# Kernel tuning notes

Hardware: AMD Instinct MI355X
Metric: run time of the kernel (lower is better)

The kernel has to match this reference:

```python
import jax, jax.numpy as jnp
import numpy as np

B, S = 1, 2048
HIDDEN = 2560
NH, NKV, HD = 32, 8, 128
GS = 128  # awq group size
ROPE_THETA = 1000000.0


def dequant_q4(qweight, scales, qzeros):
    """Unpack int4 AWQ weights -> dense [K, N] float weight.
    qweight: [K//8, N] int32, 8 nibbles packed along the input (K) dim.
    scales/qzeros: [K//GS, N]. w = (nibble - zero) * scale.
    """
    K8, N = qweight.shape
    shifts = jnp.arange(8, dtype=jnp.int32) * 4
    nib = (qweight[:, None, :] >> shifts[None, :, None]) & 0xF  # [K//8, 8, N]
    w = nib.reshape(K8 * 8, N).astype(scales.dtype)             # [K, N]
    z = jnp.repeat(qzeros.astype(scales.dtype), GS, axis=0)     # [K, N]
    s = jnp.repeat(scales, GS, axis=0)                          # [K, N]
    return (w - z) * s


def linear_q4(x, qw, sc, qz, bias=None):
    w = dequant_q4(qw, sc, qz)                     # [K, N]
    y = jnp.einsum('bsk,kn->bsn', x, w)
    return y + bias if bias is not None else y


def rotate_half(x):
    x1, x2 = jnp.split(x, 2, axis=-1)
    return jnp.concatenate([-x2, x1], axis=-1)


def apply_rope(q, k, cos, sin):
    # cos/sin: [B, S, HD] -> broadcast over heads at dim 2
    c = cos[:, :, None, :]
    s = sin[:, :, None, :]
    return q * c + rotate_half(q) * s, k * c + rotate_half(k) * s


def setup_inputs() -> dict:
    key = jax.random.key(0)
    ks = jax.random.split(key, 12)

    x = jax.random.normal(ks[0], (B, S, HIDDEN), dtype=jnp.float32)

    # genuine rotary embedding tables
    inv_freq = 1.0 / (ROPE_THETA ** (np.arange(0, HD, 2, dtype=np.float32) / HD))
    t = np.arange(S, dtype=np.float32)
    freqs = np.outer(t, inv_freq)                      # [S, HD/2]
    emb = np.concatenate([freqs, freqs], axis=-1)      # [S, HD]
    cos = jnp.asarray(np.cos(emb)[None], dtype=jnp.float32)  # [1, S, HD]
    sin = jnp.asarray(np.sin(emb)[None], dtype=jnp.float32)

    def mk_proj(kq, ksc, kz, K, N, group=GS):
        qw = jax.random.randint(kq, (K // 8, N), 0, 2**31 - 1, dtype=jnp.int32)
        sc = jax.random.normal(ksc, (K // group, N), dtype=jnp.float32) * 0.01
        qz = jax.random.randint(kz, (K // group, N), 0, 16, dtype=jnp.int32)
        return qw, sc, qz

    q_qweight, q_scales, q_qzeros = mk_proj(ks[1], ks[2], ks[3], HIDDEN, NH * HD)
    k_qweight, k_scales, k_qzeros = mk_proj(ks[4], ks[5], ks[6], HIDDEN, NKV * HD)
    v_qweight, v_scales, v_qzeros = mk_proj(ks[7], ks[8], ks[9], HIDDEN, NKV * HD)
    o_qweight, o_scales, o_qzeros = mk_proj(ks[10], ks[11], jax.random.fold_in(key, 99), NH * HD, HIDDEN)

    kb = jax.random.split(jax.random.fold_in(key, 7), 3)
    q_bias = jax.random.normal(kb[0], (NH * HD,), dtype=jnp.float32) * 0.02
    k_bias = jax.random.normal(kb[1], (NKV * HD,), dtype=jnp.float32) * 0.02
    v_bias = jax.random.normal(kb[2], (NKV * HD,), dtype=jnp.float32) * 0.02

    return dict(x=x, cos=cos, sin=sin,
                q_scales=q_scales, q_bias=q_bias,
                k_scales=k_scales, k_bias=k_bias,
                v_scales=v_scales, v_bias=v_bias,
                o_scales=o_scales,
                q_qweight=q_qweight, q_qzeros=q_qzeros,
                k_qweight=k_qweight, k_qzeros=k_qzeros,
                v_qweight=v_qweight, v_qzeros=v_qzeros,
                o_qweight=o_qweight, o_qzeros=o_qzeros)


def reference(x, cos, sin,
              q_scales, q_bias, k_scales, k_bias, v_scales, v_bias, o_scales,
              q_qweight, q_qzeros, k_qweight, k_qzeros,
              v_qweight, v_qzeros, o_qweight, o_qzeros):
    b, s, _ = x.shape
    xq = linear_q4(x, q_qweight, q_scales, q_qzeros, q_bias).reshape(b, s, NH, HD)
    xk = linear_q4(x, k_qweight, k_scales, k_qzeros, k_bias).reshape(b, s, NKV, HD)
    xv = linear_q4(x, v_qweight, v_scales, v_qzeros, v_bias).reshape(b, s, NKV, HD)

    xq, xk = apply_rope(xq, xk, cos, sin)

    # GQA: repeat KV heads to match query heads (prefill, start_pos=0)
    rep = NH // NKV
    xk = jnp.repeat(xk, rep, axis=2)   # [b, s, NH, HD]
    xv = jnp.repeat(xv, rep, axis=2)

    scale = 1.0 / jnp.sqrt(jnp.asarray(HD, dtype=xq.dtype))
    scores = jnp.einsum('bqhd,bkhd->bhqk', xq, xk) * scale  # [b, NH, s, s]
    causal = jnp.tril(jnp.ones((s, s), dtype=bool))
    scores = jnp.where(causal[None, None], scores, jnp.finfo(scores.dtype).min)
    attn = jax.nn.softmax(scores, axis=-1)
    out = jnp.einsum('bhqk,bkhd->bqhd', attn, xv).reshape(b, s, NH * HD)

    return linear_q4(out, o_qweight, o_scales, o_qzeros)  # [b, s, HIDDEN]
```

## Files before the change

### kernel.cpp

```cpp
#include <hip/hip_runtime.h>
#include <hip/hip_bf16.h>
#include <cstdint>

#define S_LEN 2048
#define HIDDEN 2560
#define NH 32
#define NKV 8
#define HD 128
#define GS 128

typedef __attribute__((ext_vector_type(8))) _Float16 half8v;
typedef __attribute__((ext_vector_type(2))) _Float16 half2v;
typedef __attribute__((ext_vector_type(4))) float f32x4;
typedef unsigned int uint;
typedef unsigned short ushort;

__device__ inline ushort f2h(float f) {
    _Float16 h = (_Float16)f;
    return __builtin_bit_cast(ushort, h);
}
__device__ inline float h2f(ushort u) {
    return (float)__builtin_bit_cast(_Float16, u);
}
__device__ inline uint pk2(ushort a, ushort b) { return (uint)a | ((uint)b << 16); }

__device__ __attribute__((always_inline)) inline void gl_lds16(const void* g, void* l) {
    __builtin_amdgcn_global_load_lds(
        (const __attribute__((address_space(1))) unsigned int*)g,
        (__attribute__((address_space(3))) unsigned int*)l, 16, 0, 0);
}

#define WAIT_LGKM0  asm volatile("s_waitcnt lgkmcnt(0)" ::: "memory")
#define WAIT_VM(N)  asm volatile("s_waitcnt vmcnt(" #N ")" ::: "memory")
#define RAW_BARRIER { __builtin_amdgcn_s_barrier(); __builtin_amdgcn_sched_barrier(0); }

__global__ __launch_bounds__(320) void xcvt_kernel(
    const float* __restrict__ X, ushort* __restrict__ Xf)
{
    const int row = blockIdx.x;
    const int t   = threadIdx.x;
    const size_t base = (size_t)row * HIDDEN + t * 8;
    float4 a = *(const float4*)&X[base];
    float4 b = *(const float4*)&X[base + 4];
    uint4 hw = {pk2(f2h(a.x), f2h(a.y)), pk2(f2h(a.z), f2h(a.w)),
                pk2(f2h(b.x), f2h(b.y)), pk2(f2h(b.z), f2h(b.w))};
    *(uint4*)&Xf[base] = hw;
}

__global__ __launch_bounds__(256) void qkv7_kernel(
    const ushort* __restrict__ Xf,
    const int* __restrict__ q_qw, const float* __restrict__ q_sc,
    const int* __restrict__ q_qz, const float* __restrict__ q_b,
    const int* __restrict__ k_qw, const float* __restrict__ k_sc,
    const int* __restrict__ k_qz, const float* __restrict__ k_b,
    const int* __restrict__ v_qw, const float* __restrict__ v_sc,
    const int* __restrict__ v_qz, const float* __restrict__ v_b,
    const float* __restrict__ cosb, const float* __restrict__ sinb,
    ushort* __restrict__ Qf, ushort* __restrict__ Kf,
    ushort* __restrict__ Vrm)
{
    __shared__ __align__(16) char LDSB[65536];
    ushort* A0 = (ushort*)(LDSB);
    ushort* A1 = (ushort*)(LDSB + 16384);
    ushort* B0 = (ushort*)(LDSB + 32768);
    ushort* B1 = (ushort*)(LDSB + 49152);

    const int t  = threadIdx.x;
    const int w  = t >> 6;
    const int l  = t & 63;
    const int lg = l >> 4;
    const int lr = l & 15;
    const int wr = w >> 1;
    const int wc = w & 1;
    const int K  = HIDDEN;

    const int bid = blockIdx.x;
    const int swz = (bid & 7) * 96 + (bid >> 3);
    const int nblk = swz % 48;
    const int m0   = (swz / 48) * 128;

    int region, nbase, Nw;
    const int* QW; const float* SC; const int* QZ; const float* BI;
    if (nblk < 32)      { region = 0; nbase = nblk * 128;        Nw = NH * HD;
                          QW = q_qw; SC = q_sc; QZ = q_qz; BI = q_b; }
    else if (nblk < 40) { region = 1; nbase = (nblk - 32) * 128; Nw = NKV * HD;
                          QW = k_qw; SC = k_sc; QZ = k_qz; BI = k_b; }
    else                { region = 2; nbase = (nblk - 40) * 128; Nw = NKV * HD;
                          QW = v_qw; SC = v_sc; QZ = v_qz; BI = v_b; }

    const int ldsAw = w * 1024;
    size_t aoff[4];
#pragma unroll
    for (int i = 0; i < 4; ++i) {
        int slot = i * 256 + t;
        int am = slot >> 3, ac = slot & 7;
        aoff[i] = (size_t)(m0 + am) * K + (size_t)((ac ^ (am & 7)) * 8);
    }
    const int bn  = t & 127;
    const int bk0 = (t >> 7) * 4;
    int bwoff[4];
#pragma unroll
    for (int j = 0; j < 4; ++j)
        bwoff[j] = (bn * 128 + (bk0 + j) * 16) ^ ((bn & 7) << 4);

    int ncm[4];
#pragma unroll
    for (int nf = 0; nf < 4; ++nf)
        ncm[nf] = wc * 32 + (nf & 1) * 16 + lr + ((nf & 2) ? 64 : 0);

    const int xorA = (lr & 7) << 4;
    int aroff[4][2], broff[4][2];
#pragma unroll
    for (int mf = 0; mf < 4; ++mf)
#pragma unroll
        for (int ks = 0; ks < 2; ++ks)
            aroff[mf][ks] = (((wr * 64 + mf * 16 + lr) * 128) + lg * 16 + ks * 64) ^ xorA;
#pragma unroll
    for (int nf = 0; nf < 4; ++nf)
#pragma unroll
        for (int ks = 0; ks < 2; ++ks)
            broff[nf][ks] = ((ncm[nf] * 128) + lg * 16 + ks * 64) ^ xorA;

    f32x4 macc[4][4];
#pragma unroll
    for (int mf = 0; mf < 4; ++mf)
#pragma unroll
        for (int nf = 0; nf < 4; ++nf) macc[mf][nf] = f32x4{0.f, 0.f, 0.f, 0.f};
    uint qr[4];
    float scf, zf;

#define QKV_QW(tile) { int g8 = (tile) * 8; int gg = (tile) >> 1; \
    _Pragma("unroll") \
    for (int j = 0; j < 4; ++j) \
        qr[j] = (uint)QW[(size_t)(g8 + bk0 + j) * Nw + nbase + bn]; \
    scf = SC[(size_t)gg * Nw + nbase + bn]; \
    zf  = (float)QZ[(size_t)gg * Nw + nbase + bn]; }

#define QKV_STAGE_A(AH, k0) { \
    gl_lds16(Xf + (k0) + aoff[0], (char*)(AH) + ldsAw); \
    gl_lds16(Xf + (k0) + aoff[1], (char*)(AH) + 4096 + ldsAw); \
    gl_lds16(Xf + (k0) + aoff[2], (char*)(AH) + 8192 + ldsAw); \
    gl_lds16(Xf + (k0) + aoff[3], (char*)(AH) + 12288 + ldsAw); }

#define QKV_BWRITE(BT) { \
    ushort sch = f2h(scf); \
    float schf = h2f(sch); \
    ushort msc = f2h(-128.0f * schf);    \
    ushort nzs = f2h(-(zf * schf)); \
    half2v S2 = {__builtin_bit_cast(_Float16, sch), __builtin_bit_cast(_Float16, sch)}; \
    half2v M2 = {__builtin_bit_cast(_Float16, msc), __builtin_bit_cast(_Float16, msc)}; \
    half2v Z2 = {__builtin_bit_cast(_Float16, nzs), __builtin_bit_cast(_Float16, nzs)}; \
    _Pragma("unroll") \
    for (int j = 0; j < 4; ++j) { \
        uint q = qr[j]; \
        uint b0 = q & 0xFFu, b1 = (q >> 8) & 0xFFu, b2 = (q >> 16) & 0xFFu, b3 = q >> 24; \
        uint e0 = 0x58005800u | ((b0 & 0xFu) << 3) | ((b0 & 0xF0u) << 15); \
        uint e1 = 0x58005800u | ((b1 & 0xFu) << 3) | ((b1 & 0xF0u) << 15); \
        uint e2 = 0x58005800u | ((b2 & 0xFu) << 3) | ((b2 & 0xF0u) << 15); \
        uint e3 = 0x58005800u | ((b3 & 0xFu) << 3) | ((b3 & 0xF0u) << 15); \
        half2v w0 = __builtin_bit_cast(half2v, e0) * S2 + M2; w0 = w0 + Z2; \
        half2v w1 = __builtin_bit_cast(half2v, e1) * S2 + M2; w1 = w1 + Z2; \
        half2v w2 = __builtin_bit_cast(half2v, e2) * S2 + M2; w2 = w2 + Z2; \
        half2v w3 = __builtin_bit_cast(half2v, e3) * S2 + M2; w3 = w3 + Z2; \
        uint4 dw = {__builtin_bit_cast(uint, w0), __builtin_bit_cast(uint, w1), \
                    __builtin_bit_cast(uint, w2), __builtin_bit_cast(uint, w3)}; \
        *(uint4*)((char*)(BT) + bwoff[j]) = dw; \
    } }

#define QKV_COMPUTE(AH, BT) { \
    _Pragma("unroll") \
    for (int ks = 0; ks < 2; ++ks) { \
        half8v av[4], bv[4]; \
        _Pragma("unroll") \
        for (int mf = 0; mf < 4; ++mf) \
            av[mf] = *(const half8v*)((const char*)(AH) + aroff[mf][ks]); \
        _Pragma("unroll") \
        for (int nf = 0; nf < 4; ++nf) \
            bv[nf] = *(const half8v*)((const char*)(BT) + broff[nf][ks]); \
        _Pragma("unroll") \
        for (int mf = 0; mf < 4; ++mf) \
            _Pragma("unroll") \
            for (int nf = 0; nf < 4; ++nf) \
                macc[mf][nf] = __builtin_amdgcn_mfma_f32_16x16x32_f16(av[mf], bv[nf], macc[mf][nf], 0, 0, 0); \
    } }

    QKV_QW(0);
    QKV_BWRITE(B0);
    QKV_STAGE_A(A0, 0);
    QKV_QW(1);
    WAIT_LGKM0;
    WAIT_VM(6);
    RAW_BARRIER;

    for (int g = 0; g < 19; ++g) {
        QKV_STAGE_A(A1, (2 * g + 1) * 64);
        QKV_COMPUTE(A0, B0);
        QKV_BWRITE(B1);
        QKV_QW(2 * g + 2);
        WAIT_LGKM0;
        WAIT_VM(6);
        RAW_BARRIER;
        QKV_STAGE_A(A0, (2 * g + 2) * 64);
        QKV_COMPUTE(A1, B1);
        QKV_BWRITE(B0);
        QKV_QW(2 * g + 3);
        WAIT_LGKM0;
        WAIT_VM(6);
        RAW_BARRIER;
    }
    QKV_STAGE_A(A1, 39 * 64);
    QKV_COMPUTE(A0, B0);
    QKV_BWRITE(B1);
    WAIT_LGKM0;
    WAIT_VM(0);
    RAW_BARRIER;
    QKV_COMPUTE(A1, B1);

#pragma unroll
    for (int nf = 0; nf < 4; ++nf) {
        float bv = BI[nbase + ncm[nf]];
#pragma unroll
        for (int mf = 0; mf < 4; ++mf)
#pragma unroll
            for (int r = 0; r < 4; ++r) macc[mf][nf][r] += bv;
    }

    if (region == 2) {
#pragma unroll
        for (int mf = 0; mf < 4; ++mf)
#pragma unroll
            for (int r = 0; r < 4; ++r) {
                int row = m0 + wr * 64 + mf * 16 + lg * 4 + r;
#pragma unroll
                for (int nf = 0; nf < 4; ++nf)
                    Vrm[(size_t)row * (NKV * HD) + nbase + ncm[nf]] = f2h(macc[mf][nf][r]);
            }
    } else {
        ushort* OF = (region == 0) ? Qf : Kf;
        const int No = (region == 0) ? NH * HD : NKV * HD;
        const float osc = (region == 0) ? 0.08838834764831845f : 1.0f;
#pragma unroll
        for (int mf = 0; mf < 4; ++mf)
#pragma unroll
            for (int r = 0; r < 4; ++r) {
                int row = m0 + wr * 64 + mf * 16 + lg * 4 + r;
                const float* cb = &cosb[(size_t)row * HD];
                const float* sb = &sinb[(size_t)row * HD];
#pragma unroll
                for (int nf = 0; nf < 2; ++nf) {
                    int d = wc * 32 + nf * 16 + lr;
                    float a = macc[mf][nf][r];
                    float b = macc[mf][nf + 2][r];
                    float o1 = (a * cb[d]      - b * sb[d])      * osc;
                    float o2 = (b * cb[d + 64] + a * sb[d + 64]) * osc;
                    OF[(size_t)row * No + nbase + d]      = f2h(o1);
                    OF[(size_t)row * No + nbase + d + 64] = f2h(o2);
                }
            }
    }
#undef QKV_QW
#undef QKV_STAGE_A
#undef QKV_BWRITE
#undef QKV_COMPUTE
}

__global__ __launch_bounds__(256) void vtrans_kernel(
    const ushort* __restrict__ Vrm, ushort* __restrict__ VfT)
{
    __shared__ ushort Ts[64][65];
    const int s0 = blockIdx.x * 64;
    const int n0 = blockIdx.y * 64;
    const int t  = threadIdx.x;
    {
        int r = t >> 2, c0 = (t & 3) * 16;
        uint4 v0 = *(const uint4*)&Vrm[(size_t)(s0 + r) * (NKV * HD) + n0 + c0];
        uint4 v1 = *(const uint4*)&Vrm[(size_t)(s0 + r) * (NKV * HD) + n0 + c0 + 8];
        const ushort* pv = (const ushort*)&v0;
#pragma unroll
        for (int j = 0; j < 8; ++j) Ts[r][c0 + j] = pv[j];
        pv = (const ushort*)&v1;
#pragma unroll
        for (int j = 0; j < 8; ++j) Ts[r][c0 + 8 + j] = pv[j];
    }
    __syncthreads();
    {
        int rn = t >> 2, cs0 = (t & 3) * 16;
        ushort ob[16];
#pragma unroll
        for (int j = 0; j < 16; ++j) ob[j] = Ts[cs0 + j][rn];
        ushort* dst = &VfT[(size_t)(n0 + rn) * S_LEN + s0 + cs0];
        *(uint4*)dst = ((uint4*)ob)[0];
        *(uint4*)(dst + 8) = ((uint4*)ob)[1];
    }
}

__global__ __launch_bounds__(256) void oproj6_kernel(
    const ushort* __restrict__ Xb, const int* __restrict__ QW,
    const float* __restrict__ SC, const int* __restrict__ QZ,
    float* __restrict__ Y)
{
    __shared__ __align__(16) char LDSB[65536];
    ushort* A0 = (ushort*)(LDSB);
    ushort* A1 = (ushort*)(LDSB + 16384);
    ushort* B0 = (ushort*)(LDSB + 32768);
    ushort* B1 = (ushort*)(LDSB + 49152);

    const int t  = threadIdx.x;
    const int w  = t >> 6;
    const int l  = t & 63;
    const int lg = l >> 4;
    const int lr = l & 15;
    const int wr = w >> 1;
    const int wc = w & 1;
    const int K  = NH * HD;
    const int N  = HIDDEN;

    const int bid = blockIdx.x;
    const int swz = (bid & 7) * 40 + (bid >> 3);
    const int n0  = (swz % 20) * 128;
    const int m0  = (swz / 20) * 128;

    const int ldsAw = w * 1024;
    size_t aoff[4];
#pragma unroll
    for (int i = 0; i < 4; ++i) {
        int slot = i * 256 + t;
        int am = slot >> 3, ac = slot & 7;
        aoff[i] = (size_t)(m0 + am) * K + (size_t)((ac ^ (am & 7)) * 8);
    }
    const int bn  = t & 127;
    const int bk0 = (t >> 7) * 4;
    int bwoff[4];
#pragma unroll
    for (int j = 0; j < 4; ++j)
        bwoff[j] = (bn * 128 + (bk0 + j) * 16) ^ ((bn & 7) << 4);

    const int xorA = (lr & 7) << 4;
    int aroff[4][2], broff[4][2];
#pragma unroll
    for (int mf = 0; mf < 4; ++mf)
#pragma unroll
        for (int ks = 0; ks < 2; ++ks)
            aroff[mf][ks] = (((wr * 64 + mf * 16 + lr) * 128) + lg * 16 + ks * 64) ^ xorA;
#pragma unroll
    for (int nf = 0; nf < 4; ++nf)
#pragma unroll
        for (int ks = 0; ks < 2; ++ks)
            broff[nf][ks] = (((wc * 64 + nf * 16 + lr) * 128) + lg * 16 + ks * 64) ^ xorA;

    f32x4 macc[4][4];
#pragma unroll
    for (int mf = 0; mf < 4; ++mf)
#pragma unroll
        for (int nf = 0; nf < 4; ++nf) macc[mf][nf] = f32x4{0.f, 0.f, 0.f, 0.f};
    uint qr[4];
    float scf, zf;

#define OP_QW(tile) { int g8 = (tile) * 8; int gg = (tile) >> 1; \
    _Pragma("unroll") \
    for (int j = 0; j < 4; ++j) \
        qr[j] = (uint)QW[(size_t)(g8 + bk0 + j) * N + n0 + bn]; \
    scf = SC[(size_t)gg * N + n0 + bn]; \
    zf  = (float)QZ[(size_t)gg * N + n0 + bn]; }

#define OP_STAGE_A(AH, k0) { \
    gl_lds16(Xb + (k0) + aoff[0], (char*)(AH) + ldsAw); \
    gl_lds16(Xb + (k0) + aoff[1], (char*)(AH) + 4096 + ldsAw); \
    gl_lds16(Xb + (k0) + aoff[2], (char*)(AH) + 8192 + ldsAw); \
    gl_lds16(Xb + (k0) + aoff[3], (char*)(AH) + 12288 + ldsAw); }

#define OP_BWRITE(BT) { \
    ushort sch = f2h(scf); \
    float schf = h2f(sch); \
    ushort msc = f2h(-128.0f * schf); \
    ushort nzs = f2h(-(zf * schf)); \
    half2v S2 = {__builtin_bit_cast(_Float16, sch), __builtin_bit_cast(_Float16, sch)}; \
    half2v M2 = {__builtin_bit_cast(_Float16, msc), __builtin_bit_cast(_Float16, msc)}; \
    half2v Z2 = {__builtin_bit_cast(_Float16, nzs), __builtin_bit_cast(_Float16, nzs)}; \
    _Pragma("unroll") \
    for (int j = 0; j < 4; ++j) { \
        uint q = qr[j]; \
        uint b0 = q & 0xFFu, b1 = (q >> 8) & 0xFFu, b2 = (q >> 16) & 0xFFu, b3 = q >> 24; \
        uint e0 = 0x58005800u | ((b0 & 0xFu) << 3) | ((b0 & 0xF0u) << 15); \
        uint e1 = 0x58005800u | ((b1 & 0xFu) << 3) | ((b1 & 0xF0u) << 15); \
        uint e2 = 0x58005800u | ((b2 & 0xFu) << 3) | ((b2 & 0xF0u) << 15); \
        uint e3 = 0x58005800u | ((b3 & 0xFu) << 3) | ((b3 & 0xF0u) << 15); \
        half2v w0 = __builtin_bit_cast(half2v, e0) * S2 + M2; w0 = w0 + Z2; \
        half2v w1 = __builtin_bit_cast(half2v, e1) * S2 + M2; w1 = w1 + Z2; \
        half2v w2 = __builtin_bit_cast(half2v, e2) * S2 + M2; w2 = w2 + Z2; \
        half2v w3 = __builtin_bit_cast(half2v, e3) * S2 + M2; w3 = w3 + Z2; \
        uint4 dw = {__builtin_bit_cast(uint, w0), __builtin_bit_cast(uint, w1), \
                    __builtin_bit_cast(uint, w2), __builtin_bit_cast(uint, w3)}; \
        *(uint4*)((char*)(BT) + bwoff[j]) = dw; \
    } }

#define OP_COMPUTE(AH, BT) { \
    _Pragma("unroll") \
    for (int ks = 0; ks < 2; ++ks) { \
        half8v av[4], bv[4]; \
        _Pragma("unroll") \
        for (int mf = 0; mf < 4; ++mf) \
            av[mf] = *(const half8v*)((const char*)(AH) + aroff[mf][ks]); \
        _Pragma("unroll") \
        for (int nf = 0; nf < 4; ++nf) \
            bv[nf] = *(const half8v*)((const char*)(BT) + broff[nf][ks]); \
        _Pragma("unroll") \
        for (int mf = 0; mf < 4; ++mf) \
            _Pragma("unroll") \
            for (int nf = 0; nf < 4; ++nf) \
                macc[mf][nf] = __builtin_amdgcn_mfma_f32_16x16x32_f16(av[mf], bv[nf], macc[mf][nf], 0, 0, 0); \
    } }

    OP_QW(0);
    OP_BWRITE(B0);
    OP_STAGE_A(A0, 0);
    OP_QW(1);
    WAIT_LGKM0;
    WAIT_VM(6);
    RAW_BARRIER;

    for (int g = 0; g < 31; ++g) {
        OP_STAGE_A(A1, (2 * g + 1) * 64);
        OP_COMPUTE(A0, B0);
        OP_BWRITE(B1);
        OP_QW(2 * g + 2);
        WAIT_LGKM0;
        WAIT_VM(6);
        RAW_BARRIER;
        OP_STAGE_A(A0, (2 * g + 2) * 64);
        OP_COMPUTE(A1, B1);
        OP_BWRITE(B0);
        OP_QW(2 * g + 3);
        WAIT_LGKM0;
        WAIT_VM(6);
        RAW_BARRIER;
    }
    OP_STAGE_A(A1, 63 * 64);
    OP_COMPUTE(A0, B0);
    OP_BWRITE(B1);
    WAIT_LGKM0;
    WAIT_VM(0);
    RAW_BARRIER;
    OP_COMPUTE(A1, B1);

#pragma unroll
    for (int mf = 0; mf < 4; ++mf)
#pragma unroll
        for (int r = 0; r < 4; ++r) {
            int row = m0 + wr * 64 + mf * 16 + lg * 4 + r;
#pragma unroll
            for (int nf = 0; nf < 4; ++nf)
                Y[(size_t)row * N + n0 + wc * 64 + nf * 16 + lr] = macc[mf][nf][r];
        }
#undef OP_QW
#undef OP_STAGE_A
#undef OP_BWRITE
#undef OP_COMPUTE
}

__global__ __launch_bounds__(256) void attn_mfma_kernel(
    const ushort* __restrict__ Qh,
    const ushort* __restrict__ Kh,
    const ushort* __restrict__ Vt,
    ushort* __restrict__ AO)
{
    __shared__ ushort KsF[32 * 128];
    __shared__ ushort Vs[128 * 32];
    __shared__ __align__(16) char PsB[4 * 1280];

    const int h  = blockIdx.x;
    const int qb = gridDim.y - 1 - blockIdx.y;
    const int s0 = qb * 64;
    const int t  = threadIdx.x;
    const int w  = t >> 6;
    const int l  = t & 63;
    const int lg = l >> 4;
    const int lr = l & 15;
    const int kvh = h >> 2;
    const int qw = s0 + w * 16;
    const int q  = qw + lr;

    half8v qf[4];
#pragma unroll
    for (int d = 0; d < 4; ++d) {
        size_t off = (size_t)q * (NH * HD) + h * HD + d * 32 + lg * 8;
        qf[d] = *(const half8v*)&Qh[off];
    }

    f32x4 o[8];
#pragma unroll
    for (int i = 0; i < 8; ++i) o[i] = f32x4{0.f, 0.f, 0.f, 0.f};
    float m = -1e30f, lsum = 0.f;
    char* pw = PsB + w * 1280;

    const int ntiles = qb * 2 + 2;
    for (int kt = 0; kt < ntiles; ++kt) {
        const int k0 = kt * 32;
#pragma unroll
        for (int i = 0; i < 2; ++i) {
            int slot = w * 128 + i * 64 + l;
            int mr = slot >> 4, c = slot & 15;
            size_t goff = (size_t)(k0 + mr) * (NKV * HD) + kvh * HD + ((c ^ (mr & 7)) * 8);
            gl_lds16(Kh + goff, (char*)KsF + (w * 128 + i * 64) * 16);
        }
#pragma unroll
        for (int i = 0; i < 2; ++i) {
            int slot = w * 128 + i * 64 + l;
            int dim = slot >> 2, c = slot & 3;
            size_t goff = (size_t)(kvh * HD + dim) * S_LEN + k0 + ((c ^ (dim & 3)) * 8);
            gl_lds16(Vt + goff, (char*)Vs + (w * 128 + i * 64) * 16);
        }
        __syncthreads();

        if (k0 <= qw + 15) {
            f32x4 s[2];
            s[0] = f32x4{0.f, 0.f, 0.f, 0.f};
            s[1] = f32x4{0.f, 0.f, 0.f, 0.f};
#pragma unroll
            for (int d = 0; d < 4; ++d) {
#pragma unroll
                for (int nt2 = 0; nt2 < 2; ++nt2) {
                    int row = nt2 * 16 + lr;
                    int off = row * 256 + ((d * 64 + lg * 16) ^ ((row & 7) << 4));
                    half8v kf = *(const half8v*)((char*)KsF + off);
                    s[nt2] = __builtin_amdgcn_mfma_f32_16x16x32_f16(kf, qf[d], s[nt2], 0, 0, 0);
                }
            }
            float sv[8];
#pragma unroll
            for (int nt2 = 0; nt2 < 2; ++nt2)
#pragma unroll
                for (int r = 0; r < 4; ++r) {
                    int kv = k0 + nt2 * 16 + lg * 4 + r;
                    sv[nt2 * 4 + r] = (kv <= q) ? s[nt2][r] : -1e30f;
                }
            float mx = sv[0];
#pragma unroll
            for (int j = 1; j < 8; ++j) mx = fmaxf(mx, sv[j]);
            mx = fmaxf(mx, __shfl_xor(mx, 16));
            mx = fmaxf(mx, __shfl_xor(mx, 32));
            float mnew = fmaxf(m, mx);
            float resc = __expf(m - mnew);
            m = mnew;
            float p[8], ps = 0.f;
#pragma unroll
            for (int j = 0; j < 8; ++j) { p[j] = __expf(sv[j] - mnew); ps += p[j]; }
            ps += __shfl_xor(ps, 16);
            ps += __shfl_xor(ps, 32);
            lsum = lsum * resc + ps;
#pragma unroll
            for (int dt = 0; dt < 8; ++dt)
#pragma unroll
                for (int r = 0; r < 4; ++r) o[dt][r] *= resc;
            uint2 w0 = {pk2(f2h(p[0]), f2h(p[1])), pk2(f2h(p[2]), f2h(p[3]))};
            uint2 w1 = {pk2(f2h(p[4]), f2h(p[5])), pk2(f2h(p[6]), f2h(p[7]))};
            *(uint2*)(pw + lr * 80 + lg * 8)      = w0;
            *(uint2*)(pw + lr * 80 + 32 + lg * 8) = w1;
            asm volatile("s_waitcnt lgkmcnt(0)" ::: "memory");
            half8v pf = *(const half8v*)(pw + lr * 80 + lg * 16);
#pragma unroll
            for (int dt = 0; dt < 8; ++dt) {
                int dim = dt * 16 + lr;
                half8v vf = *(const half8v*)((char*)Vs + dim * 64 + ((lg * 16) ^ ((dim & 3) << 4)));
                o[dt] = __builtin_amdgcn_mfma_f32_16x16x32_f16(vf, pf, o[dt], 0, 0, 0);
            }
        }
        __syncthreads();
    }

    float inv = 1.f / lsum;
    ushort* dst = &AO[(size_t)q * (NH * HD) + h * HD];
#pragma unroll
    for (int dt = 0; dt < 8; ++dt) {
        uint2 ov = {pk2(f2h(o[dt][0] * inv), f2h(o[dt][1] * inv)),
                    pk2(f2h(o[dt][2] * inv), f2h(o[dt][3] * inv))};
        *(uint2*)(dst + dt * 16 + lg * 4) = ov;
    }
}

extern "C" void kernel_launch(void* const* d_in, const int* in_sizes, int n_in,
                              void* d_out, int out_size, void* d_ws, size_t ws_size,
                              hipStream_t stream)
{
    const float* x    = (const float*)d_in[0];
    const float* cosb = (const float*)d_in[1];
    const float* sinb = (const float*)d_in[2];
    const float* q_sc = (const float*)d_in[3];
    const float* q_b  = (const float*)d_in[4];
    const float* k_sc = (const float*)d_in[5];
    const float* k_b  = (const float*)d_in[6];
    const float* v_sc = (const float*)d_in[7];
    const float* v_b  = (const float*)d_in[8];
    const float* o_sc = (const float*)d_in[9];
    const int* q_qw   = (const int*)d_in[10];
    const int* q_qz   = (const int*)d_in[11];
    const int* k_qw   = (const int*)d_in[12];
    const int* k_qz   = (const int*)d_in[13];
    const int* v_qw   = (const int*)d_in[14];
    const int* v_qz   = (const int*)d_in[15];
    const int* o_qw   = (const int*)d_in[16];
    const int* o_qz   = (const int*)d_in[17];
    float* out = (float*)d_out;

    char* ws = (char*)d_ws;
    ushort* Xf   = (ushort*)ws;
    ushort* AOf  = (ushort*)ws;
    ushort* Qf   = (ushort*)(ws + (size_t)16 * 1024 * 1024);
    ushort* Kf   = (ushort*)(ws + (size_t)32 * 1024 * 1024);
    ushort* Vrm  = (ushort*)(ws + (size_t)36 * 1024 * 1024);
    ushort* VfT  = (ushort*)(ws + (size_t)40 * 1024 * 1024);

    xcvt_kernel<<<S_LEN, 320, 0, stream>>>(x, Xf);

    qkv7_kernel<<<768, 256, 0, stream>>>(
        Xf,
        q_qw, q_sc, q_qz, q_b,
        k_qw, k_sc, k_qz, k_b,
        v_qw, v_sc, v_qz, v_b,
        cosb, sinb, Qf, Kf, Vrm);

    vtrans_kernel<<<dim3(S_LEN / 64, (NKV * HD) / 64), 256, 0, stream>>>(Vrm, VfT);

    attn_mfma_kernel<<<dim3(NH, S_LEN / 64), 256, 0, stream>>>(Qf, Kf, VfT, AOf);

    oproj6_kernel<<<320, 256, 0, stream>>>(
        AOf, o_qw, o_sc, o_qz, out);
}
```

Baseline: 265.6 us.

## Double-buffer K/V tiles in attention kernel to overlap loads with compute

Splits the attention kernel's shared K and V tiles into two buffers and prefetches the next 32-key tile via direct global-to-LDS loads while the current tile's QK, softmax and PV MFMAs run. The loop is unrolled by two with a vmcnt wait and barrier after each tile, replacing the old load, sync, compute, sync pattern. This aims to hide global memory latency in the attention loop. It doubles the K/V LDS footprint, which may reduce occupancy. ntiles is always even, so the unroll by two is safe.

```diff
diff --git a/kernel.cpp b/kernel.cpp
--- a/kernel.cpp
+++ b/kernel.cpp
@@ -464,8 +464,10 @@
     const ushort* __restrict__ Vt,
     ushort* __restrict__ AO)
 {
-    __shared__ ushort KsF[32 * 128];
-    __shared__ ushort Vs[128 * 32];
+    __shared__ ushort Ks0[32 * 128];
+    __shared__ ushort Ks1[32 * 128];
+    __shared__ ushort Vs0[128 * 32];
+    __shared__ ushort Vs1[128 * 32];
     __shared__ __align__(16) char PsB[4 * 1280];
 
     const int h  = blockIdx.x;
@@ -493,79 +495,92 @@
     float m = -1e30f, lsum = 0.f;
     char* pw = PsB + w * 1280;
 
+#define ATTN_STAGE(KB, VB, k0) { \
+    _Pragma("unroll") \
+    for (int i = 0; i < 2; ++i) { \
+        int slot = w * 128 + i * 64 + l; \
+        int mr = slot >> 4, c = slot & 15; \
+        size_t goff = (size_t)((k0) + mr) * (NKV * HD) + kvh * HD + ((c ^ (mr & 7)) * 8); \
+        gl_lds16(Kh + goff, (char*)(KB) + (w * 128 + i * 64) * 16); \
+    } \
+    _Pragma("unroll") \
+    for (int i = 0; i < 2; ++i) { \
+        int slot = w * 128 + i * 64 + l; \
+        int dim = slot >> 2, c = slot & 3; \
+        size_t goff = (size_t)(kvh * HD + dim) * S_LEN + (k0) + ((c ^ (dim & 3)) * 8); \
+        gl_lds16(Vt + goff, (char*)(VB) + (w * 128 + i * 64) * 16); \
+    } }
+
+#define ATTN_TILE(KSF, VSS, k0) \
+    if ((k0) <= qw + 15) { \
+        f32x4 s_[2]; \
+        s_[0] = f32x4{0.f, 0.f, 0.f, 0.f}; \
+        s_[1] = f32x4{0.f, 0.f, 0.f, 0.f}; \
+        _Pragma("unroll") \
+        for (int d = 0; d < 4; ++d) { \
+            _Pragma("unroll") \
+            for (int nt2 = 0; nt2 < 2; ++nt2) { \
+                int row = nt2 * 16 + lr; \
+                int off = row * 256 + ((d * 64 + lg * 16) ^ ((row & 7) << 4)); \
+                half8v kf = *(const half8v*)((const char*)(KSF) + off); \
+                s_[nt2] = __builtin_amdgcn_mfma_f32_16x16x32_f16(kf, qf[d], s_[nt2], 0, 0, 0); \
+            } \
+        } \
+        float sv[8]; \
+        _Pragma("unroll") \
+        for (int nt2 = 0; nt2 < 2; ++nt2) \
+            _Pragma("unroll") \
+            for (int r = 0; r < 4; ++r) { \
+                int kv = (k0) + nt2 * 16 + lg * 4 + r; \
+                sv[nt2 * 4 + r] = (kv <= q) ? s_[nt2][r] : -1e30f; \
+            } \
+        float mx = sv[0]; \
+        _Pragma("unroll") \
+        for (int j = 1; j < 8; ++j) mx = fmaxf(mx, sv[j]); \
+        mx = fmaxf(mx, __shfl_xor(mx, 16)); \
+        mx = fmaxf(mx, __shfl_xor(mx, 32)); \
+        float mnew = fmaxf(m, mx); \
+        float resc = __expf(m - mnew); \
+        m = mnew; \
+        float p_[8], ps = 0.f; \
+        _Pragma("unroll") \
+        for (int j = 0; j < 8; ++j) { p_[j] = __expf(sv[j] - mnew); ps += p_[j]; } \
+        ps += __shfl_xor(ps, 16); \
+        ps += __shfl_xor(ps, 32); \
+        lsum = lsum * resc + ps; \
+        _Pragma("unroll") \
+        for (int dt = 0; dt < 8; ++dt) \
+            _Pragma("unroll") \
+            for (int r = 0; r < 4; ++r) o[dt][r] *= resc; \
+        uint2 w0_ = {pk2(f2h(p_[0]), f2h(p_[1])), pk2(f2h(p_[2]), f2h(p_[3]))}; \
+        uint2 w1_ = {pk2(f2h(p_[4]), f2h(p_[5])), pk2(f2h(p_[6]), f2h(p_[7]))}; \
+        *(uint2*)(pw + lr * 80 + lg * 8)      = w0_; \
+        *(uint2*)(pw + lr * 80 + 32 + lg * 8) = w1_; \
+        asm volatile("s_waitcnt lgkmcnt(0)" ::: "memory"); \
+        half8v pf = *(const half8v*)(pw + lr * 80 + lg * 16); \
+        _Pragma("unroll") \
+        for (int dt = 0; dt < 8; ++dt) { \
+            int dim = dt * 16 + lr; \
+            half8v vf = *(const half8v*)((const char*)(VSS) + dim * 64 + ((lg * 16) ^ ((dim & 3) << 4))); \
+            o[dt] = __builtin_amdgcn_mfma_f32_16x16x32_f16(vf, pf, o[dt], 0, 0, 0); \
+        } \
+    }
+
     const int ntiles = qb * 2 + 2;
-    for (int kt = 0; kt < ntiles; ++kt) {
-        const int k0 = kt * 32;
-#pragma unroll
-        for (int i = 0; i < 2; ++i) {
-            int slot = w * 128 + i * 64 + l;
-            int mr = slot >> 4, c = slot & 15;
-            size_t goff = (size_t)(k0 + mr) * (NKV * HD) + kvh * HD + ((c ^ (mr & 7)) * 8);
-            gl_lds16(Kh + goff, (char*)KsF + (w * 128 + i * 64) * 16);
-        }
-#pragma unroll
-        for (int i = 0; i < 2; ++i) {
-            int slot = w * 128 + i * 64 + l;
-            int dim = slot >> 2, c = slot & 3;
-            size_t goff = (size_t)(kvh * HD + dim) * S_LEN + k0 + ((c ^ (dim & 3)) * 8);
-            gl_lds16(Vt + goff, (char*)Vs + (w * 128 + i * 64) * 16);
-        }
-        __syncthreads();
-
-        if (k0 <= qw + 15) {
-            f32x4 s[2];
-            s[0] = f32x4{0.f, 0.f, 0.f, 0.f};
-            s[1] = f32x4{0.f, 0.f, 0.f, 0.f};
-#pragma unroll
-            for (int d = 0; d < 4; ++d) {
-#pragma unroll
-                for (int nt2 = 0; nt2 < 2; ++nt2) {
-                    int row = nt2 * 16 + lr;
-                    int off = row * 256 + ((d * 64 + lg * 16) ^ ((row & 7) << 4));
-                    half8v kf = *(const half8v*)((char*)KsF + off);
-                    s[nt2] = __builtin_amdgcn_mfma_f32_16x16x32_f16(kf, qf[d], s[nt2], 0, 0, 0);
-                }
-            }
-            float sv[8];
-#pragma unroll
-            for (int nt2 = 0; nt2 < 2; ++nt2)
-#pragma unroll
-                for (int r = 0; r < 4; ++r) {
-                    int kv = k0 + nt2 * 16 + lg * 4 + r;
-                    sv[nt2 * 4 + r] = (kv <= q) ? s[nt2][r] : -1e30f;
-                }
-            float mx = sv[0];
-#pragma unroll
-            for (int j = 1; j < 8; ++j) mx = fmaxf(mx, sv[j]);
-            mx = fmaxf(mx, __shfl_xor(mx, 16));
-            mx = fmaxf(mx, __shfl_xor(mx, 32));
-            float mnew = fmaxf(m, mx);
-            float resc = __expf(m - mnew);
-            m = mnew;
-            float p[8], ps = 0.f;
-#pragma unroll
-            for (int j = 0; j < 8; ++j) { p[j] = __expf(sv[j] - mnew); ps += p[j]; }
-            ps += __shfl_xor(ps, 16);
-            ps += __shfl_xor(ps, 32);
-            lsum = lsum * resc + ps;
-#pragma unroll
-            for (int dt = 0; dt < 8; ++dt)
-#pragma unroll
-                for (int r = 0; r < 4; ++r) o[dt][r] *= resc;
-            uint2 w0 = {pk2(f2h(p[0]), f2h(p[1])), pk2(f2h(p[2]), f2h(p[3]))};
-            uint2 w1 = {pk2(f2h(p[4]), f2h(p[5])), pk2(f2h(p[6]), f2h(p[7]))};
-            *(uint2*)(pw + lr * 80 + lg * 8)      = w0;
-            *(uint2*)(pw + lr * 80 + 32 + lg * 8) = w1;
-            asm volatile("s_waitcnt lgkmcnt(0)" ::: "memory");
-            half8v pf = *(const half8v*)(pw + lr * 80 + lg * 16);
-#pragma unroll
-            for (int dt = 0; dt < 8; ++dt) {
-                int dim = dt * 16 + lr;
-                half8v vf = *(const half8v*)((char*)Vs + dim * 64 + ((lg * 16) ^ ((dim & 3) << 4)));
-                o[dt] = __builtin_amdgcn_mfma_f32_16x16x32_f16(vf, pf, o[dt], 0, 0, 0);
-            }
-        }
-        __syncthreads();
+
+    ATTN_STAGE(Ks0, Vs0, 0);
+    WAIT_VM(0);
+    RAW_BARRIER;
+
+    for (int kt = 0; kt < ntiles; kt += 2) {
+        if (kt + 1 < ntiles) ATTN_STAGE(Ks1, Vs1, (kt + 1) * 32);
+        ATTN_TILE(Ks0, Vs0, kt * 32);
+        WAIT_VM(0);
+        RAW_BARRIER;
+        if (kt + 2 < ntiles) ATTN_STAGE(Ks0, Vs0, (kt + 2) * 32);
+        ATTN_TILE(Ks1, Vs1, (kt + 1) * 32);
+        WAIT_VM(0);
+        RAW_BARRIER;
     }
 
     float inv = 1.f / lsum;
@@ -576,6 +591,8 @@
                     pk2(f2h(o[dt][2] * inv), f2h(o[dt][3] * inv))};
         *(uint2*)(dst + dt * 16 + lg * 4) = ov;
     }
+#undef ATTN_STAGE
+#undef ATTN_TILE
 }
 
 extern "C" void kernel_launch(void* const* d_in, const int* in_sizes, int n_in,
```

New measurement: 264.5 us. Within noise of the previous version (-0.4%).
